# Optimization experiments

Hardware: AMD Instinct MI355X
Metric: run time of the kernel (lower is better)

## Reference

```python
import jax, jax.numpy as jnp
import numpy as np


def setup_inputs() -> dict:
    key = jax.random.key(0)
    k1, k2 = jax.random.split(key)
    B, S, H, D = 4, 2048, 12, 64
    v = jax.random.normal(k1, (B, S, H, D), dtype=jnp.float32)
    # learned per-head positional weights, sorted ascending along last dim
    # (mirrors torch.sort(torch.randn(H, S), dim=-1)[0])
    w = jnp.sort(jax.random.normal(k2, (H, S), dtype=jnp.float32), axis=-1)
    return {"v": v, "w": w}


def reference(v, w):
    # PositionalBias._naive
    # v: [B, S, H, D]; w: [H, S_max]
    B, S, H, D = v.shape
    seq_len = S - 2  # v[:, 1:-1] is the non-special-token span
    w_ = w[:, :seq_len]  # [H, seq_len]
    # _construct_bias builds bias[h, l, j] = w[h, |l - j|] (symmetric Toeplitz)
    pos = jnp.arange(seq_len)
    idx = jnp.abs(pos[:, None] - pos[None, :])  # [seq_len, seq_len]
    bias = w_[:, idx]  # [H, seq_len, seq_len]
    # zero-pad one row/col on each side -> [H, S, S]
    bias = jnp.pad(bias, ((0, 0), (1, 1), (1, 1)))
    # z_pb: [1, S, H]
    z_pb = jnp.sum(bias, axis=-1).T[None, :, :]
    # pbv: [B, S, H, D]
    pbv = jnp.einsum('nlhd,hlj->njhd', v, bias)
    return (pbv, z_pb)
```

## Files before the change

### kernel.cpp

```cpp
#include <hip/hip_runtime.h>
#include <hip/hip_bf16.h>


typedef short short8 __attribute__((ext_vector_type(8)));
typedef float floatx4 __attribute__((ext_vector_type(4)));

typedef const __attribute__((address_space(1))) void gvoid_t;
typedef __attribute__((address_space(3))) void lvoid_t;

__device__ __forceinline__ unsigned short f2bf(float f) {
  union { __hip_bfloat16 b; unsigned short u; } cv;
  cv.b = __float2bfloat16(f);
  return cv.u;
}

__global__ __launch_bounds__(256) void prep_kernel(const float* __restrict__ v,
                                                   const float* __restrict__ w,
                                                   unsigned short* __restrict__ vb,
                                                   float* __restrict__ zout) {
  __shared__ float smem[64 * 65];
  const int lt = blockIdx.x;
  const int h  = blockIdx.y;
  const int n  = blockIdx.z;
  const int tid = threadIdx.x;

  if (lt == 32) {
    if (n != 0) return;
    float* wv  = smem;
    float* pfx = smem + 2048;
    __shared__ float wsum[4];
    const float* wh = w + (size_t)h * 2048;
    for (int i = tid; i < 2048; i += 256) wv[i] = (i < 2046) ? wh[i] : 0.f;
    __syncthreads();
    const int base = tid * 8;
    float run0 = 0.f;
    #pragma unroll
    for (int k = 0; k < 8; ++k) run0 += wv[base + k];
    float x = run0;
    #pragma unroll
    for (int d = 1; d < 64; d <<= 1) {
      float y = __shfl_up(x, d);
      if ((tid & 63) >= d) x += y;
    }
    if ((tid & 63) == 63) wsum[tid >> 6] = x;
    __syncthreads();
    const int wid = tid >> 6;
    float woff = 0.f;
    #pragma unroll
    for (int u = 0; u < 3; ++u) { float t = wsum[u]; if (u < wid) woff += t; }
    float pr = x + woff - run0;
    #pragma unroll
    for (int k = 0; k < 8; ++k) { pr += wv[base + k]; pfx[base + k] = pr; }
    __syncthreads();
    for (int i = tid; i < 2046; i += 256) {
      float z = pfx[i] + pfx[2045 - i] - wv[0];
      zout[(size_t)(i + 1) * 12 + h] = z;
    }
    if (tid == 0) { zout[h] = 0.f; zout[(size_t)2047 * 12 + h] = 0.f; }
    return;
  }

  float (*tile)[65] = (float(*)[65])smem;
  const int l0 = lt * 64;
  {
    const int d  = tid & 63;
    const int r0 = tid >> 6;
    #pragma unroll
    for (int rr = 0; rr < 16; ++rr) {
      int ll = r0 * 16 + rr;
      tile[ll][d] = v[(((size_t)n * 2048 + (l0 + ll)) * 12 + h) * 64 + d];
    }
  }
  __syncthreads();
  {
    const int d = tid >> 2;
    const int q = tid & 3;
    const int nd = n * 64 + d;
    const int sw = nd & 7;
    unsigned short buf[16] __attribute__((aligned(16)));
    #pragma unroll
    for (int jj = 0; jj < 16; ++jj) {
      int l = l0 + q * 16 + jj;
      float f = tile[q * 16 + jj][d];
      buf[jj] = (l == 0 || l == 2047) ? (unsigned short)0 : f2bf(f);
    }
    unsigned short* dstrow = vb + ((size_t)h * 256 + nd) * 2048 + l0;
    int c0 = (2 * q) ^ sw, c1 = (2 * q + 1) ^ sw;
    *(uint4*)(dstrow + c0 * 8) = *(const uint4*)&buf[0];
    *(uint4*)(dstrow + c1 * 8) = *(const uint4*)&buf[8];
  }
}

__global__ __launch_bounds__(256, 3) void gemm_kernel(const float* __restrict__ w,
                                                      const unsigned short* __restrict__ vb,
                                                      float* __restrict__ out) {
  __shared__ __attribute__((aligned(16))) short Tls[8 * 2184];
  __shared__ __attribute__((aligned(16))) short vt[2][64][64];

  const int jt  = blockIdx.x;
  const int ndt = blockIdx.y;
  const int h   = blockIdx.z;
  const int tid = threadIdx.x;
  const int lane = tid & 63;
  const int wid  = tid >> 6;
  const int wm = wid >> 1, wn = wid & 1;
  const int lm = lane & 15, quad = lane >> 4;
  const int jb = jt * 128;
  const int nd0 = ndt * 64;
  const unsigned short* vbp = vb + (size_t)h * 256 * 2048;

  auto issue_dma = [&](int l0, int b) {
    #pragma unroll
    for (int u = 0; u < 2; ++u) {
      int e = wid * 2 + u;
      const unsigned short* g = vbp + (size_t)(nd0 + e * 8 + (lane >> 3)) * 2048 + l0 + (lane & 7) * 8;
      __builtin_amdgcn_global_load_lds((gvoid_t*)g, (lvoid_t*)&vt[b][e * 8][0], 16, 0, 0);
    }
  };

  issue_dma(0, 0);

  const float* wh = w + (size_t)h * 2048;
  for (int g = tid; g < 8 * 273; g += 256) {
    int c  = g / 273;
    int p8 = (g - c * 273) * 8;
    unsigned short buf[8] __attribute__((aligned(16)));
    #pragma unroll
    for (int i = 0; i < 8; ++i) {
      int t = 127 + jb - (p8 + i) - c;
      int a = t < 0 ? -t : t;
      buf[i] = (a <= 2045) ? f2bf(wh[a]) : (unsigned short)0;
    }
    *(short8*)&Tls[c * 2184 + p8] = *(const short8*)buf;
  }
  __syncthreads();

  floatx4 acc[4][2];
  #pragma unroll
  for (int ma = 0; ma < 4; ++ma)
    #pragma unroll
    for (int na = 0; na < 2; ++na)
      acc[ma][na] = (floatx4){0.f, 0.f, 0.f, 0.f};

  const int pbase = 127 + quad * 8 - wm * 64 - lm;
  auto load_af = [&](int g16, int l0) -> short8 {
    int p0 = l0 + g16 + pbase;
    int c  = p0 & 7;
    return *(const short8*)&Tls[c * 2184 + (p0 - c)];
  };

  short8 a4 = load_af(-48, 0);
  short8 a5 = load_af(-32, 0);

  #pragma unroll 2
  for (int t = 0; t < 32; ++t) {
    const int l0 = t * 64;
    const int b  = t & 1;
    short8 afr[6];
    afr[0] = a4; afr[1] = a5;
    afr[2] = load_af(-16, l0);
    afr[3] = load_af(0,   l0);
    afr[4] = load_af(16,  l0);
    afr[5] = load_af(32,  l0);
    a4 = afr[4]; a5 = afr[5];

    asm volatile("s_waitcnt vmcnt(0)" ::: "memory");
    __syncthreads();
    if (t < 31) issue_dma(l0 + 64, b ^ 1);

    #pragma unroll
    for (int kc = 0; kc < 2; ++kc) {
      short8 bfr[2];
      #pragma unroll
      for (int na = 0; na < 2; ++na) {
        int row  = wn * 32 + na * 16 + lm;
        int slot = (kc * 4 + quad) ^ (lm & 7);
        bfr[na] = *(const short8*)&vt[b][row][slot * 8];
      }
      #pragma unroll
      for (int ma = 0; ma < 4; ++ma) {
        short8 af = afr[(kc ? 5 : 3) - ma];
        #pragma unroll
        for (int na = 0; na < 2; ++na)
          acc[ma][na] = __builtin_amdgcn_mfma_f32_16x16x32_bf16(af, bfr[na], acc[ma][na], 0, 0, 0);
      }
    }
  }

  const int jw  = jb + wm * 64;
  const int ndw = nd0 + wn * 32;
  #pragma unroll
  for (int ma = 0; ma < 4; ++ma) {
    #pragma unroll
    for (int na = 0; na < 2; ++na) {
      floatx4 c = acc[ma][na];
      int ndv = ndw + na * 16 + lm;
      int n = ndv >> 6, d = ndv & 63;
      #pragma unroll
      for (int r = 0; r < 4; ++r) {
        int j = jw + ma * 16 + quad * 4 + r;
        float val = (j == 0 || j == 2047) ? 0.f : c[r];
        out[(size_t)n * 1572864 + (size_t)j * 768 + h * 64 + d] = val;
      }
    }
  }
}

extern "C" void kernel_launch(void* const* d_in, const int* in_sizes, int n_in,
                              void* d_out, int out_size, void* d_ws, size_t ws_size,
                              hipStream_t stream) {
  const float* v = (const float*)d_in[0];
  const float* w = (const float*)d_in[1];
  float* out = (float*)d_out;
  unsigned short* vb = (unsigned short*)d_ws;

  prep_kernel<<<dim3(33, 12, 4), 256, 0, stream>>>(v, w, vb, out + 6291456);
  gemm_kernel<<<dim3(16, 4, 12), 256, 0, stream>>>(w, vb, out);
}
```

Before: 123.7 us.

## Stream V operand directly from global into registers, widen Toeplitz tile per wave

Replaces the LDS double-buffered global_load_lds staging of the V operand with per-wave direct register loads prefetched one step ahead. Each wave now owns a 16-column strip across all 128 output rows, so it issues 8 MFMAs per B fragment. The Toeplitz A fragments are kept in a sliding register window. Also vectorizes the prep kernel's input loads to float4, drops the XOR swizzle in the workspace layout, and remaps the grid so that blocks sharing a head are adjacent. The aim is to remove per-iteration barriers and LDS traffic for B. The cost is more registers and uncoalesced, cache-dependent global loads.

```diff
diff --git a/kernel.cpp b/kernel.cpp
--- a/kernel.cpp
+++ b/kernel.cpp
@@ -5,8 +5,7 @@
 typedef short short8 __attribute__((ext_vector_type(8)));
 typedef float floatx4 __attribute__((ext_vector_type(4)));
 
-typedef const __attribute__((address_space(1))) void gvoid_t;
-typedef __attribute__((address_space(3))) void lvoid_t;
+#define TL 2280
 
 __device__ __forceinline__ unsigned short f2bf(float f) {
   union { __hip_bfloat16 b; unsigned short u; } cv;
@@ -63,12 +62,16 @@
   float (*tile)[65] = (float(*)[65])smem;
   const int l0 = lt * 64;
   {
-    const int d  = tid & 63;
-    const int r0 = tid >> 6;
+    const int row = tid >> 2;
+    const int cq  = (tid & 3) * 16;
+    const float* src = v + (((size_t)n * 2048 + (l0 + row)) * 12 + h) * 64 + cq;
     #pragma unroll
-    for (int rr = 0; rr < 16; ++rr) {
-      int ll = r0 * 16 + rr;
-      tile[ll][d] = v[(((size_t)n * 2048 + (l0 + ll)) * 12 + h) * 64 + d];
+    for (int u = 0; u < 4; ++u) {
+      float4 f4 = *(const float4*)(src + u * 4);
+      tile[row][cq + u * 4 + 0] = f4.x;
+      tile[row][cq + u * 4 + 1] = f4.y;
+      tile[row][cq + u * 4 + 2] = f4.z;
+      tile[row][cq + u * 4 + 3] = f4.w;
     }
   }
   __syncthreads();
@@ -76,7 +79,6 @@
     const int d = tid >> 2;
     const int q = tid & 3;
     const int nd = n * 64 + d;
-    const int sw = nd & 7;
     unsigned short buf[16] __attribute__((aligned(16)));
     #pragma unroll
     for (int jj = 0; jj < 16; ++jj) {
@@ -84,46 +86,36 @@
       float f = tile[q * 16 + jj][d];
       buf[jj] = (l == 0 || l == 2047) ? (unsigned short)0 : f2bf(f);
     }
-    unsigned short* dstrow = vb + ((size_t)h * 256 + nd) * 2048 + l0;
-    int c0 = (2 * q) ^ sw, c1 = (2 * q + 1) ^ sw;
-    *(uint4*)(dstrow + c0 * 8) = *(const uint4*)&buf[0];
-    *(uint4*)(dstrow + c1 * 8) = *(const uint4*)&buf[8];
+    unsigned short* dst = vb + ((size_t)h * 256 + nd) * 2048 + l0 + q * 16;
+    *(uint4*)dst       = *(const uint4*)&buf[0];
+    *(uint4*)(dst + 8) = *(const uint4*)&buf[8];
   }
 }
 
 __global__ __launch_bounds__(256, 3) void gemm_kernel(const float* __restrict__ w,
                                                       const unsigned short* __restrict__ vb,
                                                       float* __restrict__ out) {
-  __shared__ __attribute__((aligned(16))) short Tls[8 * 2184];
-  __shared__ __attribute__((aligned(16))) short vt[2][64][64];
+  __shared__ __attribute__((aligned(16))) short Tls[8 * TL];
 
-  const int jt  = blockIdx.x;
-  const int ndt = blockIdx.y;
-  const int h   = blockIdx.z;
+  const int ndt = blockIdx.x & 3;
+  const int h   = blockIdx.x >> 2;
+  const int jt  = blockIdx.y;
   const int tid = threadIdx.x;
   const int lane = tid & 63;
   const int wid  = tid >> 6;
-  const int wm = wid >> 1, wn = wid & 1;
   const int lm = lane & 15, quad = lane >> 4;
   const int jb = jt * 128;
-  const int nd0 = ndt * 64;
-  const unsigned short* vbp = vb + (size_t)h * 256 * 2048;
+  const int strip = ndt * 64 + wid * 16;
 
-  auto issue_dma = [&](int l0, int b) {
-    #pragma unroll
-    for (int u = 0; u < 2; ++u) {
-      int e = wid * 2 + u;
-      const unsigned short* g = vbp + (size_t)(nd0 + e * 8 + (lane >> 3)) * 2048 + l0 + (lane & 7) * 8;
-      __builtin_amdgcn_global_load_lds((gvoid_t*)g, (lvoid_t*)&vt[b][e * 8][0], 16, 0, 0);
-    }
-  };
+  const unsigned short* brow = vb + ((size_t)h * 256 + strip + lm) * 2048 + quad * 8;
 
-  issue_dma(0, 0);
+  short8 b0 = *(const short8*)(brow);
+  short8 b1 = *(const short8*)(brow + 32);
 
   const float* wh = w + (size_t)h * 2048;
-  for (int g = tid; g < 8 * 273; g += 256) {
-    int c  = g / 273;
-    int p8 = (g - c * 273) * 8;
+  for (int g = tid; g < 8 * (TL / 8); g += 256) {
+    int c  = g / (TL / 8);
+    int p8 = (g - c * (TL / 8)) * 8;
     unsigned short buf[8] __attribute__((aligned(16)));
     #pragma unroll
     for (int i = 0; i < 8; ++i) {
@@ -131,77 +123,59 @@
       int a = t < 0 ? -t : t;
       buf[i] = (a <= 2045) ? f2bf(wh[a]) : (unsigned short)0;
     }
-    *(short8*)&Tls[c * 2184 + p8] = *(const short8*)buf;
+    *(short8*)&Tls[c * TL + p8] = *(const short8*)buf;
   }
   __syncthreads();
 
-  floatx4 acc[4][2];
-  #pragma unroll
-  for (int ma = 0; ma < 4; ++ma)
-    #pragma unroll
-    for (int na = 0; na < 2; ++na)
-      acc[ma][na] = (floatx4){0.f, 0.f, 0.f, 0.f};
-
-  const int pbase = 127 + quad * 8 - wm * 64 - lm;
-  auto load_af = [&](int g16, int l0) -> short8 {
-    int p0 = l0 + g16 + pbase;
-    int c  = p0 & 7;
-    return *(const short8*)&Tls[c * 2184 + (p0 - c)];
+  const int pbase = 127 + quad * 8 - lm;
+  auto load_af = [&](int p0) -> short8 {
+    int c = p0 & 7;
+    return *(const short8*)&Tls[c * TL + (p0 - c)];
   };
 
-  short8 a4 = load_af(-48, 0);
-  short8 a5 = load_af(-32, 0);
+  short8 afr[10];
+  #pragma unroll
+  for (int i = 0; i < 10; ++i) afr[i] = load_af((i - 7) * 16 + pbase);
 
-  #pragma unroll 2
+  floatx4 acc[8];
+  #pragma unroll
+  for (int ma = 0; ma < 8; ++ma) acc[ma] = (floatx4){0.f, 0.f, 0.f, 0.f};
+
+  #pragma unroll 4
   for (int t = 0; t < 32; ++t) {
     const int l0 = t * 64;
-    const int b  = t & 1;
-    short8 afr[6];
-    afr[0] = a4; afr[1] = a5;
-    afr[2] = load_af(-16, l0);
-    afr[3] = load_af(0,   l0);
-    afr[4] = load_af(16,  l0);
-    afr[5] = load_af(32,  l0);
-    a4 = afr[4]; a5 = afr[5];
-
-    asm volatile("s_waitcnt vmcnt(0)" ::: "memory");
-    __syncthreads();
-    if (t < 31) issue_dma(l0 + 64, b ^ 1);
+    const int tn = (t < 31) ? t + 1 : 31;
+    short8 nb0 = *(const short8*)(brow + tn * 64);
+    short8 nb1 = *(const short8*)(brow + tn * 64 + 32);
+    short8 na0 = load_af(l0 + 64 - 16 + pbase);
+    short8 na1 = load_af(l0 + 64      + pbase);
+    short8 na2 = load_af(l0 + 64 + 16 + pbase);
+    short8 na3 = load_af(l0 + 64 + 32 + pbase);
 
     #pragma unroll
-    for (int kc = 0; kc < 2; ++kc) {
-      short8 bfr[2];
-      #pragma unroll
-      for (int na = 0; na < 2; ++na) {
-        int row  = wn * 32 + na * 16 + lm;
-        int slot = (kc * 4 + quad) ^ (lm & 7);
-        bfr[na] = *(const short8*)&vt[b][row][slot * 8];
-      }
-      #pragma unroll
-      for (int ma = 0; ma < 4; ++ma) {
-        short8 af = afr[(kc ? 5 : 3) - ma];
-        #pragma unroll
-        for (int na = 0; na < 2; ++na)
-          acc[ma][na] = __builtin_amdgcn_mfma_f32_16x16x32_bf16(af, bfr[na], acc[ma][na], 0, 0, 0);
-      }
-    }
+    for (int ma = 0; ma < 8; ++ma)
+      acc[ma] = __builtin_amdgcn_mfma_f32_16x16x32_bf16(afr[7 - ma], b0, acc[ma], 0, 0, 0);
+    #pragma unroll
+    for (int ma = 0; ma < 8; ++ma)
+      acc[ma] = __builtin_amdgcn_mfma_f32_16x16x32_bf16(afr[9 - ma], b1, acc[ma], 0, 0, 0);
+
+    #pragma unroll
+    for (int i = 0; i < 6; ++i) afr[i] = afr[i + 4];
+    afr[6] = na0; afr[7] = na1; afr[8] = na2; afr[9] = na3;
+    b0 = nb0; b1 = nb1;
   }
 
-  const int jw  = jb + wm * 64;
-  const int ndw = nd0 + wn * 32;
+  const int ndv = strip + lm;
+  const int n = ndv >> 6, d = ndv & 63;
+  float* obase = out + (size_t)n * 1572864 + (size_t)h * 64 + d;
   #pragma unroll
-  for (int ma = 0; ma < 4; ++ma) {
+  for (int ma = 0; ma < 8; ++ma) {
+    floatx4 c = acc[ma];
     #pragma unroll
-    for (int na = 0; na < 2; ++na) {
-      floatx4 c = acc[ma][na];
-      int ndv = ndw + na * 16 + lm;
-      int n = ndv >> 6, d = ndv & 63;
-      #pragma unroll
-      for (int r = 0; r < 4; ++r) {
-        int j = jw + ma * 16 + quad * 4 + r;
-        float val = (j == 0 || j == 2047) ? 0.f : c[r];
-        out[(size_t)n * 1572864 + (size_t)j * 768 + h * 64 + d] = val;
-      }
+    for (int r = 0; r < 4; ++r) {
+      int j = jb + ma * 16 + quad * 4 + r;
+      float val = (j == 0 || j == 2047) ? 0.f : c[r];
+      obase[(size_t)j * 768] = val;
     }
   }
 }
@@ -215,5 +189,5 @@
   unsigned short* vb = (unsigned short*)d_ws;
 
   prep_kernel<<<dim3(33, 12, 4), 256, 0, stream>>>(v, w, vb, out + 6291456);
-  gemm_kernel<<<dim3(16, 4, 12), 256, 0, stream>>>(w, vb, out);
+  gemm_kernel<<<dim3(48, 16, 1), 256, 0, stream>>>(w, vb, out);
 }
```

After: 126.7 us. +2.5%, slower.
